# Kernel tuning notes

Hardware: AMD Instinct MI355X
Metric: run time of the kernel (lower is better)

The kernel has to match this reference:

```python
import jax, jax.numpy as jnp
import numpy as np

# cfg constants (ProposalLayerSoft.__init__)
GRID_SIZE = jnp.array([8000.0, 8000.0, 2000.0], dtype=jnp.float32)   # MULTI_PERSON.SPACE_SIZE (mm)
CUBE_SIZE = jnp.array([128.0, 128.0, 64.0], dtype=jnp.float32)       # MULTI_PERSON.INITIAL_CUBE_SIZE
GRID_CENTER = jnp.array([0.0, 0.0, 300.0], dtype=jnp.float32)        # MULTI_PERSON.SPACE_CENTER
NUM_CAND = 10                                                         # MULTI_PERSON.MAX_PEOPLE_NUM
THRESHOLD = 0.3                                                       # MULTI_PERSON.THRESHOLD


def setup_inputs() -> dict:
    key = jax.random.key(0)
    # root heatmap cube in [0,1): [B, X, Y, Z]
    root_cubes = jax.random.uniform(key, (32, 128, 128, 64), dtype=jnp.float32)
    return {"root_cubes": root_cubes}


def _nms_topk(x):
    """3x3x3 max-pool peak suppression + top-k (repo's nms()).
    x: [B, X, Y, Z] -> (values [B,K], unravel_index [B,K,3] float)."""
    B, X, Y, Z = x.shape
    pooled = jax.lax.reduce_window(
        x, -jnp.inf, jax.lax.max,
        window_dimensions=(1, 3, 3, 3),
        window_strides=(1, 1, 1, 1),
        padding=[(0, 0), (1, 1), (1, 1), (1, 1)],
    )
    peaks = jnp.where(x == pooled, x, 0.0)           # keep only local maxima
    flat = peaks.reshape(B, X * Y * Z)
    topk_values, topk_index = jax.lax.top_k(flat, NUM_CAND)
    # C-order unravel (matches repo's get_index)
    ix = topk_index // (Y * Z)
    iy = (topk_index % (Y * Z)) // Z
    iz = topk_index % Z
    idx = jnp.stack([ix, iy, iz], axis=-1).astype(jnp.float32)  # [B, K, 3]
    return topk_values, idx


def reference(root_cubes):
    x = jax.lax.stop_gradient(root_cubes)  # original calls .detach()
    topk_values, topk_index = _nms_topk(x)
    # get_real_loc: voxel index -> world coords (mm)
    loc = topk_index / (CUBE_SIZE - 1.0) * GRID_SIZE + GRID_CENTER - GRID_SIZE / 2.0
    conf = (topk_values > THRESHOLD).astype(jnp.float32) - 1.0  # col 3
    grid_centers = jnp.concatenate(
        [loc, conf[..., None], topk_values[..., None]], axis=-1
    )  # [B, K, 5]: (x, y, z, valid_flag, score)
    return grid_centers
```

## Files before the change

kernel.cpp:

```cpp
#include <hip/hip_runtime.h>
#include <stdint.h>


#define TPB 256
#define NK 10
#define TX 10
#define BLOCKS_PER_B (4 * TX)
#define WCAP 512
typedef unsigned long long u64;

__device__ __forceinline__ u64 bfly_max_u64(u64 v) {
#pragma unroll
  for (int off = 1; off < 64; off <<= 1) {
    u64 o = __shfl_xor(v, off, 64);
    v = (o > v) ? o : v;
  }
  return v;
}

__global__ __launch_bounds__(TPB, 4) void peaks_topk(
    const float* __restrict__ in, u64* __restrict__ part) {
  __shared__ u64 cand[4][WCAP];
  __shared__ u64 wtop[4 * NK];
  const int tid = threadIdx.x;
  const int w = tid >> 6, lane = tid & 63;
  const int xi = lane >> 2, zq = lane & 3;
  const int tx = blockIdx.x, b = blockIdx.z;
  const int seg = blockIdx.y * 4 + w;
  const int x0 = tx * 14 - 1;
  const int gx = x0 + xi;
  const int cx = min(127, max(0, gx));
  const int y0 = seg * 8;
  const bool emit_ok = (xi >= 1) && (xi <= 14) && (gx <= 127);
  const float* __restrict__ col =
      in + ((size_t)b << 20) + ((size_t)cx << 13) + (zq << 4);

  int wcnt = 0;
  float vC[16], vN[16], zmP[16], zmC[16], zmN[16];

  auto loadv = [&](int y, float* v) {
    const int cy = min(127, max(0, y));
    const float4* p = (const float4*)(col + ((size_t)cy << 6));
    float4 a = p[0], bb = p[1], c = p[2], d = p[3];
    v[0] = a.x;  v[1] = a.y;  v[2] = a.z;  v[3] = a.w;
    v[4] = bb.x; v[5] = bb.y; v[6] = bb.z; v[7] = bb.w;
    v[8] = c.x;  v[9] = c.y;  v[10] = c.z; v[11] = c.w;
    v[12] = d.x; v[13] = d.y; v[14] = d.z; v[15] = d.w;
  };
  auto zmcalc = [&](const float* v, float* zm) {
    float vl = __shfl_up(v[15], 1, 64);
    float vr = __shfl_down(v[0], 1, 64);
    vl = (zq == 0) ? -1e30f : vl;
    vr = (zq == 3) ? -1e30f : vr;
    zm[0] = fmaxf(vl, fmaxf(v[0], v[1]));
#pragma unroll
    for (int j = 1; j < 15; ++j)
      zm[j] = fmaxf(v[j - 1], fmaxf(v[j], v[j + 1]));
    zm[15] = fmaxf(v[14], fmaxf(v[15], vr));
  };

  loadv(y0 - 1, vC);
  zmcalc(vC, zmP);
  loadv(y0, vC);
  zmcalc(vC, zmC);

#pragma unroll
  for (int t = 0; t < 8; ++t) {
    const int y = y0 + t;
    loadv(y + 1, vN);
    zmcalc(vN, zmN);
#pragma unroll
    for (int j = 0; j < 16; ++j) {
      float ym = fmaxf(zmP[j], fmaxf(zmC[j], zmN[j]));
      float l = __shfl_up(ym, 4, 64);
      float r = __shfl_down(ym, 4, 64);
      float m27 = fmaxf(ym, fmaxf(l, r));
      float v = vC[j];
      const bool pred = emit_ok && (v >= m27);
      u64 mask = __ballot(pred);
      if (pred) {
        unsigned g = ((unsigned)gx << 13) | ((unsigned)y << 6) |
                     (unsigned)((zq << 4) + j);
        u64 key = ((u64)__float_as_uint(v) << 32) | (u64)(unsigned)(~g);
        int ofs = __builtin_amdgcn_mbcnt_hi(
            (unsigned)(mask >> 32),
            __builtin_amdgcn_mbcnt_lo((unsigned)mask, 0));
        int slot = wcnt + ofs;
        if (slot < WCAP) cand[w][slot] = key;
      }
      wcnt += (int)__popcll(mask);
    }
#pragma unroll
    for (int j = 0; j < 16; ++j) {
      zmP[j] = zmC[j];
      zmC[j] = zmN[j];
      vC[j] = vN[j];
    }
  }

  __builtin_amdgcn_s_waitcnt(0);
  const int count = min(wcnt, WCAP);
  u64 c[WCAP / 64];
#pragma unroll
  for (int i = 0; i < WCAP / 64; ++i) {
    int idx = lane + (i << 6);
    c[i] = (idx < count) ? cand[w][idx] : 0;
  }
  u64 mine = 0;
#pragma unroll 1
  for (int r = 0; r < NK; ++r) {
    u64 best = c[0];
#pragma unroll
    for (int i = 1; i < WCAP / 64; ++i) best = (c[i] > best) ? c[i] : best;
    u64 m = bfly_max_u64(best);
    if (m != 0 && best == m) {
#pragma unroll
      for (int i = 0; i < WCAP / 64; ++i)
        if (c[i] == m) c[i] = 0;
    }
    if (lane == r) mine = m;
  }
  if (lane < NK) wtop[w * NK + lane] = mine;
  __syncthreads();

  if (w == 0) {
    u64 c0 = (lane < 4 * NK) ? wtop[lane] : 0;
    u64 mv = 0;
#pragma unroll 1
    for (int r = 0; r < NK; ++r) {
      u64 m = bfly_max_u64(c0);
      if (m != 0 && c0 == m) c0 = 0;
      if (lane == r) mv = m;
    }
    if (lane < NK) {
      const int bi = blockIdx.y * TX + tx;
      part[((size_t)b * BLOCKS_PER_B + bi) * NK + lane] = mv;
    }
  }
}

__global__ __launch_bounds__(TPB) void final_select(
    const u64* __restrict__ part, float* __restrict__ out) {
  __shared__ u64 cand[512];
  __shared__ u64 red4[4];
  const int tid = threadIdx.x;
  const int b = blockIdx.x;
  const int w = tid >> 6, lane = tid & 63;
  const int NKEY = BLOCKS_PER_B * NK;

  const u64* __restrict__ src = part + (size_t)b * NKEY;
  for (int i = tid; i < 512; i += TPB) cand[i] = (i < NKEY) ? src[i] : 0;
  __syncthreads();

  for (int r = 0; r < NK; ++r) {
    u64 best = 0;
    int slot = -1;
#pragma unroll
    for (int k = 0; k < 2; ++k) {
      int i = tid + k * TPB;
      if (cand[i] > best) { best = cand[i]; slot = i; }
    }
    u64 wm = bfly_max_u64(best);
    if (lane == 0) red4[w] = wm;
    __syncthreads();
    u64 win = red4[0];
#pragma unroll
    for (int k = 1; k < 4; ++k) win = (red4[k] > win) ? red4[k] : win;
    if (win != 0 && best == win && slot >= 0) cand[slot] = 0;
    if (tid == 0) {
      float val = 0.0f;
      unsigned g = 0u;
      if (win != 0) {
        val = __uint_as_float((unsigned)(win >> 32));
        g = ~((unsigned)win);
      }
      float fx = (float)(g >> 13) * (8000.0f / 127.0f) - 4000.0f;
      float fy = (float)((g >> 6) & 127u) * (8000.0f / 127.0f) - 4000.0f;
      float fz = (float)(g & 63u) * (2000.0f / 63.0f) - 700.0f;
      float conf = (val > 0.3f) ? 0.0f : -1.0f;
      float* o = out + ((size_t)b * NK + r) * 5;
      o[0] = fx; o[1] = fy; o[2] = fz; o[3] = conf; o[4] = val;
    }
    __syncthreads();
  }
}

extern "C" void kernel_launch(void* const* d_in, const int* in_sizes, int n_in,
                              void* d_out, int out_size, void* d_ws, size_t ws_size,
                              hipStream_t stream) {
  const float* in = (const float*)d_in[0];
  float* out = (float*)d_out;
  u64* part = (u64*)d_ws;

  const int B = in_sizes[0] >> 20;
  dim3 gridA(TX, 4, (unsigned)B);
  peaks_topk<<<gridA, dim3(TPB), 0, stream>>>(in, part);
  final_select<<<dim3((unsigned)B), dim3(TPB), 0, stream>>>(part, out);
}
```

Baseline: 219.4 us.

## Remap lanes x-fastest, use DPP row shifts for x-neighbors, prefetch rows two ahead

```diff
diff --git a/kernel.cpp b/kernel.cpp
--- a/kernel.cpp
+++ b/kernel.cpp
@@ -18,13 +18,22 @@
   return v;
 }
 
+__device__ __forceinline__ float dpp_nbr_a(float v) {
+  return __int_as_float(__builtin_amdgcn_update_dpp(
+      0, __float_as_int(v), 0x101, 0xF, 0xF, true));
+}
+__device__ __forceinline__ float dpp_nbr_b(float v) {
+  return __int_as_float(__builtin_amdgcn_update_dpp(
+      0, __float_as_int(v), 0x111, 0xF, 0xF, true));
+}
+
 __global__ __launch_bounds__(TPB, 4) void peaks_topk(
     const float* __restrict__ in, u64* __restrict__ part) {
   __shared__ u64 cand[4][WCAP];
   __shared__ u64 wtop[4 * NK];
   const int tid = threadIdx.x;
   const int w = tid >> 6, lane = tid & 63;
-  const int xi = lane >> 2, zq = lane & 3;
+  const int xi = lane & 15, zq = lane >> 4;
   const int tx = blockIdx.x, b = blockIdx.z;
   const int seg = blockIdx.y * 4 + w;
   const int x0 = tx * 14 - 1;
@@ -36,7 +45,7 @@
       in + ((size_t)b << 20) + ((size_t)cx << 13) + (zq << 4);
 
   int wcnt = 0;
-  float vC[16], vN[16], zmP[16], zmC[16], zmN[16];
+  float vb[3][16], zmb[3][16];
 
   auto loadv = [&](int y, float* v) {
     const int cy = min(127, max(0, y));
@@ -48,8 +57,8 @@
     v[12] = d.x; v[13] = d.y; v[14] = d.z; v[15] = d.w;
   };
   auto zmcalc = [&](const float* v, float* zm) {
-    float vl = __shfl_up(v[15], 1, 64);
-    float vr = __shfl_down(v[0], 1, 64);
+    float vl = __shfl_up(v[15], 16, 64);
+    float vr = __shfl_down(v[0], 16, 64);
     vl = (zq == 0) ? -1e30f : vl;
     vr = (zq == 3) ? -1e30f : vr;
     zm[0] = fmaxf(vl, fmaxf(v[0], v[1]));
@@ -59,21 +68,26 @@
     zm[15] = fmaxf(v[14], fmaxf(v[15], vr));
   };
 
-  loadv(y0 - 1, vC);
-  zmcalc(vC, zmP);
-  loadv(y0, vC);
-  zmcalc(vC, zmC);
+  loadv(y0 - 1, vb[2]);
+  loadv(y0, vb[0]);
+  loadv(y0 + 1, vb[1]);
+  zmcalc(vb[2], zmb[2]);
+  zmcalc(vb[0], zmb[0]);
 
 #pragma unroll
   for (int t = 0; t < 8; ++t) {
     const int y = y0 + t;
-    loadv(y + 1, vN);
-    zmcalc(vN, zmN);
+    if (t < 7) loadv(y + 2, vb[(t + 2) % 3]);
+    zmcalc(vb[(t + 1) % 3], zmb[(t + 1) % 3]);
+    const float* vC = vb[t % 3];
+    const float* zmP = zmb[(t + 2) % 3];
+    const float* zmC = zmb[t % 3];
+    const float* zmN = zmb[(t + 1) % 3];
 #pragma unroll
     for (int j = 0; j < 16; ++j) {
       float ym = fmaxf(zmP[j], fmaxf(zmC[j], zmN[j]));
-      float l = __shfl_up(ym, 4, 64);
-      float r = __shfl_down(ym, 4, 64);
+      float l = dpp_nbr_a(ym);
+      float r = dpp_nbr_b(ym);
       float m27 = fmaxf(ym, fmaxf(l, r));
       float v = vC[j];
       const bool pred = emit_ok && (v >= m27);
@@ -90,12 +104,6 @@
       }
       wcnt += (int)__popcll(mask);
     }
-#pragma unroll
-    for (int j = 0; j < 16; ++j) {
-      zmP[j] = zmC[j];
-      zmC[j] = zmN[j];
-      vC[j] = vN[j];
-    }
   }
 
   __builtin_amdgcn_s_waitcnt(0);
```

New measurement: 215.1 us. 1.02x faster.
